# Optimization experiments

Hardware: AMD Instinct MI355X
Metric: run time of the kernel (lower is better)

## Reference

```python
import jax, jax.numpy as jnp
import numpy as np

GAMMA = 2
EPS = 1e-8  # torch F.cosine_similarity norm clamp


def setup_inputs() -> dict:
    key = jax.random.key(0)
    k1, k2, k3 = jax.random.split(key, 3)
    b, c, h, w = 32, 256, 32, 32
    x = jax.random.normal(k1, (b, c, h, w), dtype=jnp.float32)
    # 1x1 conv transform_net (num_layers=1): weight (c_out, c_in), bias (c_out,)
    conv_w = jax.random.normal(k2, (c, c), dtype=jnp.float32) / np.sqrt(c)
    conv_b = jax.random.normal(k3, (c,), dtype=jnp.float32) * 0.01
    return {"x": x, "conv_w": conv_w, "conv_b": conv_b}


def reference(x, conv_w, conv_b):
    b, c, h, w = x.shape
    hw = h * w
    xf = x.reshape(b, c, hw)  # (b, c, hw)
    # cosine similarity: normalize channels once, then a single GEMM
    norm = jnp.sqrt(jnp.sum(xf * xf, axis=1, keepdims=True))
    xn = xf / jnp.maximum(norm, EPS)
    sim = jnp.einsum('bcq,bck->bqk', xn, xn)  # (b, hw, hw)
    sim = jax.nn.relu(sim) ** GAMMA
    # 1x1 conv transform
    t = jnp.einsum('oc,bck->bok', conv_w, xf) + conv_b[None, :, None]  # (b, c, hw)
    # weighted aggregation: out[b, c, q] = sum_k sim[b, q, k] * t[b, c, k]
    out = jnp.einsum('bqk,bck->bcq', sim, t)
    return out.reshape(b, c, h, w)
```

## Files before the change

kernel.cpp:

```cpp
#include <hip/hip_runtime.h>
#include <math.h>

#define B 32
#define C 256
#define HW 1024

typedef __attribute__((ext_vector_type(8))) short bf16x8;
typedef __attribute__((ext_vector_type(4))) float f32x4;

__device__ __forceinline__ unsigned short f2bf(float f) {
    unsigned int u = __float_as_uint(f);
    u += 0x7fffu + ((u >> 16) & 1u);
    return (unsigned short)(u >> 16);
}

__device__ __forceinline__ void gload16(const void* g, void* l) {
    __builtin_amdgcn_global_load_lds(
        (const __attribute__((address_space(1))) unsigned int*)g,
        (__attribute__((address_space(3))) unsigned int*)l, 16, 0, 0);
}

__global__ __launch_bounds__(256) void prepn_kernel(const float* __restrict__ x,
                                                    float* __restrict__ norm,
                                                    unsigned short* __restrict__ xnT) {
    __shared__ float xt[256][65];
    __shared__ float psum[4][64];
    __shared__ float rn[64];
    const int t = threadIdx.x;
    const int q0 = blockIdx.x * 64, b = blockIdx.y;
    const float* xb = x + (size_t)b * C * HW + q0;
#pragma unroll
    for (int p = 0; p < 16; ++p) {
        int u = p * 256 + t;
        int c = u >> 4, q4 = (u & 15) * 4;
        float4 v = *(const float4*)(xb + (size_t)c * HW + q4);
        xt[c][q4] = v.x; xt[c][q4 + 1] = v.y; xt[c][q4 + 2] = v.z; xt[c][q4 + 3] = v.w;
    }
    __syncthreads();
    {
        int cb = t >> 6, q = t & 63;
        float s = 0.f;
#pragma unroll
        for (int cc = 0; cc < 64; ++cc) {
            float v = xt[cb * 64 + cc][q];
            s += v * v;
        }
        psum[cb][q] = s;
    }
    __syncthreads();
    if (t < 64) {
        float s = psum[0][t] + psum[1][t] + psum[2][t] + psum[3][t];
        float n = fmaxf(sqrtf(s), 1e-8f);
        norm[b * HW + q0 + t] = n;
        rn[t] = 1.f / n;
    }
    __syncthreads();
    unsigned short* xrow = xnT + ((size_t)b * HW + q0) * C;
#pragma unroll
    for (int p = 0; p < 16; ++p) {
        int q = p * 4 + (t >> 6);
        float rnq = rn[q];
#pragma unroll
        for (int i = 0; i < 4; ++i) {
            int c = (t & 63) + 64 * i;
            xrow[(size_t)q * C + c] = f2bf(xt[c][q] * rnq);
        }
    }
}

__global__ __launch_bounds__(256) void castw_kernel(const float* __restrict__ w,
                                                    unsigned short* __restrict__ wb) {
    int i = (blockIdx.x * 256 + threadIdx.x) * 4;
    float4 v = *(const float4*)(w + i);
    unsigned long long pk = (unsigned long long)f2bf(v.x) |
                            ((unsigned long long)f2bf(v.y) << 16) |
                            ((unsigned long long)f2bf(v.z) << 32) |
                            ((unsigned long long)f2bf(v.w) << 48);
    *(unsigned long long*)(wb + i) = pk;
}

__global__ __launch_bounds__(256) void tgemm_kernel(
    const unsigned short* __restrict__ A, const unsigned short* __restrict__ Bm,
    unsigned short* __restrict__ Cb, const float* __restrict__ bias,
    const float* __restrict__ norm) {
    __shared__ unsigned short Asub[128 * 64];
    __shared__ unsigned short Bsub[128 * 64];
    const int t = threadIdx.x;
    const int bz = blockIdx.z;
    const int m0 = blockIdx.y * 128, n0 = blockIdx.x * 128;

    const int ug = ((t & 7) ^ ((t >> 3) & 7)) * 16;
    const char* gA = (const char*)A + (size_t)(m0 + (t >> 3)) * (C * 2) + ug;
    const char* gB = (const char*)(Bm + (size_t)bz * HW * C) +
                     (size_t)(n0 + (t >> 3)) * (C * 2) + ug;
    char* lA = (char*)Asub + t * 16;
    char* lB = (char*)Bsub + t * 16;
    const int rowStep = 32 * C * 2;

    const int lane = t & 63;
    const int wid = t >> 6;
    const int wr = wid >> 1, wc = wid & 1;
    const int lr = lane & 15, hi = lane >> 4;
    int rowA[4], rowB[4], sb[2];
#pragma unroll
    for (int i = 0; i < 4; ++i) rowA[i] = (wr * 64 + i * 16 + lr) * 128;
#pragma unroll
    for (int j = 0; j < 4; ++j) rowB[j] = (wc * 64 + j * 16 + lr) * 128;
#pragma unroll
    for (int kk = 0; kk < 2; ++kk) sb[kk] = ((hi + 4 * kk) ^ (lr & 7)) * 16;

    f32x4 acc[4][4];
#pragma unroll
    for (int i = 0; i < 4; ++i)
#pragma unroll
        for (int j = 0; j < 4; ++j) acc[i][j] = (f32x4)(0.f);

#pragma unroll
    for (int p = 0; p < 4; ++p) {
        gload16(gA + p * rowStep, lA + p * 4096);
        gload16(gB + p * rowStep, lB + p * 4096);
    }
    for (int ks = 0; ks < 4; ++ks) {
        __syncthreads();
#pragma unroll
        for (int kk = 0; kk < 2; ++kk) {
            bf16x8 av[4], bv[4];
#pragma unroll
            for (int i = 0; i < 4; ++i)
                av[i] = *(const bf16x8*)((const char*)Asub + rowA[i] + sb[kk]);
#pragma unroll
            for (int j = 0; j < 4; ++j)
                bv[j] = *(const bf16x8*)((const char*)Bsub + rowB[j] + sb[kk]);
#pragma unroll
            for (int i = 0; i < 4; ++i)
#pragma unroll
                for (int j = 0; j < 4; ++j)
                    acc[i][j] = __builtin_amdgcn_mfma_f32_16x16x32_bf16(
                        av[i], bv[j], acc[i][j], 0, 0, 0);
        }
        __syncthreads();
        if (ks + 1 < 4) {
            const char* gA2 = gA + (size_t)(ks + 1) * 128;
            const char* gB2 = gB + (size_t)(ks + 1) * 128;
#pragma unroll
            for (int p = 0; p < 4; ++p) {
                gload16(gA2 + p * rowStep, lA + p * 4096);
                gload16(gB2 + p * rowStep, lB + p * 4096);
            }
        }
    }
    const int mb = m0 + wr * 64 + hi * 4;
    const int nb = n0 + wc * 64 + lr;
    unsigned short* Cp = Cb + (size_t)bz * C * HW;
    float nrm[4];
#pragma unroll
    for (int j = 0; j < 4; ++j) nrm[j] = norm[bz * HW + nb + j * 16];
#pragma unroll
    for (int i = 0; i < 4; ++i)
#pragma unroll
        for (int r = 0; r < 4; ++r) {
            int m = mb + i * 16 + r;
            float bbv = bias[m];
#pragma unroll
            for (int j = 0; j < 4; ++j)
                Cp[(size_t)m * HW + nb + j * 16] = f2bf(acc[i][j][r] * nrm[j] + bbv);
        }
}

__global__ __launch_bounds__(512, 4) void fused_kernel(
    const unsigned short* __restrict__ xnT,
    const unsigned short* __restrict__ tb,
    float* __restrict__ out) {
    __shared__ unsigned short XQ[64 * 256];
    __shared__ unsigned short XK0[128 * 64];
    __shared__ unsigned short XK1[128 * 64];
    __shared__ unsigned short SS[64 * 128];
    const int t = threadIdx.x;
    const int wgid = blockIdx.x;
    const int xcd = wgid & 7, g = wgid >> 3;
    const int qt = g & 15, bh = g >> 4;
    const int b = bh * 8 + xcd;
    const int qg0 = qt * 64;

    const int lane = t & 63;
    const int wid = t >> 6;
    const int lr = lane & 15, hi = lane >> 4;
    const int qh = wid & 1, kq = wid >> 1;

    const char* xq_g = (const char*)(xnT + ((size_t)b * HW + qg0) * C);
    const char* xk_gb = (const char*)(xnT + (size_t)b * HW * C);
    const char* t_gb = (const char*)(tb + (size_t)b * C * HW);

    auto stage_xk = [&](int kg0, int cch, char* dst) {
#pragma unroll
        for (int p = 0; p < 2; ++p) {
            int u = p * 512 + t;
            int k = u >> 3, s = u & 7;
            int sp = s ^ (k & 7);
            gload16(xk_gb + (size_t)(kg0 + k) * 512 + cch * 128 + sp * 16,
                    dst + u * 16);
        }
    };

#pragma unroll
    for (int p = 0; p < 4; ++p) {
        int u = p * 512 + t;
        int q = u >> 5, s = u & 31;
        int sp = (s & 16) | ((s & 15) ^ (q & 15));
        gload16(xq_g + (size_t)q * 512 + sp * 16, (char*)XQ + (size_t)u * 16);
    }
    stage_xk(0, 0, (char*)XK0);

    f32x4 oacc[2][4];
#pragma unroll
    for (int i = 0; i < 2; ++i)
#pragma unroll
        for (int j = 0; j < 4; ++j) oacc[i][j] = (f32x4)(0.f);

    for (int kt = 0; kt < 8; ++kt) {
        const int kg0 = kt * 128;
        f32x4 sacc[2][2];
#pragma unroll
        for (int i = 0; i < 2; ++i)
#pragma unroll
            for (int j = 0; j < 2; ++j) sacc[i][j] = (f32x4)(0.f);

#pragma unroll
        for (int cch = 0; cch < 4; ++cch) {
            __syncthreads();
            char* nbuf = (cch & 1) ? (char*)XK0 : (char*)XK1;
            if (cch < 3) stage_xk(kg0, cch + 1, nbuf);
            else         stage_xk(kt < 7 ? kg0 + 128 : kg0, 0, (char*)XK0);
            const char* xk = (cch & 1) ? (const char*)XK1 : (const char*)XK0;
#pragma unroll
            for (int cs = 0; cs < 2; ++cs) {
                bf16x8 av[2], bv[2];
#pragma unroll
                for (int i = 0; i < 2; ++i) {
                    int krow = kq * 32 + i * 16 + lr;
                    int off = (cs * 64 + hi * 16) ^ ((krow & 7) << 4);
                    av[i] = *(const bf16x8*)(xk + krow * 128 + off);
                }
#pragma unroll
                for (int j = 0; j < 2; ++j) {
                    int qrow = qh * 32 + j * 16 + lr;
                    int off = (cch * 128 + cs * 64 + hi * 16) ^ ((qrow & 15) << 4);
                    bv[j] = *(const bf16x8*)((const char*)XQ + qrow * 512 + off);
                }
#pragma unroll
                for (int i = 0; i < 2; ++i)
#pragma unroll
                    for (int j = 0; j < 2; ++j)
                        sacc[i][j] = __builtin_amdgcn_mfma_f32_16x16x32_bf16(
                            av[i], bv[j], sacc[i][j], 0, 0, 0);
            }
        }

#pragma unroll
        for (int i = 0; i < 2; ++i)
#pragma unroll
            for (int j = 0; j < 2; ++j) {
                int q = qh * 32 + j * 16 + lr;
                int kb = kq * 32 + i * 16 + hi * 4;
                unsigned long long pk = 0;
#pragma unroll
                for (int r = 0; r < 4; ++r) {
                    float v = fmaxf(sacc[i][j][r], 0.f);
                    v = v * v;
                    pk |= (unsigned long long)f2bf(v) << (16 * r);
                }
                int off = (kb * 2) ^ ((q & 15) << 4);
                *(unsigned long long*)((char*)SS + q * 256 + off) = pk;
            }
        __syncthreads();

        bf16x8 tt[2][4];
#pragma unroll
        for (int i = 0; i < 2; ++i)
#pragma unroll
            for (int kc = 0; kc < 4; ++kc)
                tt[i][kc] = *(const bf16x8*)(
                    t_gb + (size_t)(wid * 32 + i * 16 + lr) * 2048 +
                    (kg0 + kc * 32 + hi * 8) * 2);
#pragma unroll
        for (int kc = 0; kc < 4; ++kc) {
            bf16x8 bv[4];
#pragma unroll
            for (int j = 0; j < 4; ++j) {
                int qrow = j * 16 + lr;
                int off = (kc * 64 + hi * 16) ^ ((qrow & 15) << 4);
                bv[j] = *(const bf16x8*)((const char*)SS + qrow * 256 + off);
            }
#pragma unroll
            for (int i = 0; i < 2; ++i)
#pragma unroll
                for (int j = 0; j < 4; ++j)
                    oacc[i][j] = __builtin_amdgcn_mfma_f32_16x16x32_bf16(
                        tt[i][kc], bv[j], oacc[i][j], 0, 0, 0);
        }
    }

#pragma unroll
    for (int i = 0; i < 2; ++i)
#pragma unroll
        for (int r = 0; r < 4; ++r) {
            int c = wid * 32 + i * 16 + hi * 4 + r;
            float* op = out + ((size_t)b * C + c) * HW + qg0 + lr;
#pragma unroll
            for (int j = 0; j < 4; ++j) op[j * 16] = oacc[i][j][r];
        }
}

extern "C" void kernel_launch(void* const* d_in, const int* in_sizes, int n_in,
                              void* d_out, int out_size, void* d_ws, size_t ws_size,
                              hipStream_t stream) {
    const float* x    = (const float*)d_in[0];
    const float* w    = (const float*)d_in[1];
    const float* bias = (const float*)d_in[2];
    float* out = (float*)d_out;

    char* ws = (char*)d_ws;
    float* norm         = (float*)ws;
    unsigned short* wbf = (unsigned short*)(ws + (128 << 10));
    unsigned short* xnT = (unsigned short*)(ws + (256 << 10));
    unsigned short* tb  = (unsigned short*)(ws + (256 << 10) + (16u << 20));

    hipLaunchKernelGGL(prepn_kernel, dim3(HW / 64, B), dim3(256), 0, stream,
                       x, norm, xnT);
    hipLaunchKernelGGL(castw_kernel, dim3(C * C / 1024), dim3(256), 0, stream, w, wbf);
    hipLaunchKernelGGL(tgemm_kernel, dim3(HW / 128, C / 128, B), dim3(256), 0, stream,
                       wbf, xnT, tb, bias, norm);
    hipLaunchKernelGGL(fused_kernel, dim3((HW / 64) * B), dim3(512), 0, stream,
                       xnT, tb, out);
}
```

Before: 78.94 us.

## Load key tiles straight from global into registers, drop LDS double-buffer for keys

The sim GEMM stage no longer stages key rows of xnT through two LDS buffers with per-chunk barriers. Each wave now loads its 16 key rows across all 256 channels directly from global into registers and runs MFMAs against the resident query tile. The work split changes from a 2x4 wave grid to one 16-key slice per wave, and the many __syncthreads are replaced by a few explicit waitcnt+barrier points. This saves LDS space and synchronisation, but adds register pressure and exposes uncoalesced global load latency with no prefetch overlap.

Result: slower. 93.65 us (+18.6%).

```diff
diff --git a/kernel.cpp b/kernel.cpp
--- a/kernel.cpp
+++ b/kernel.cpp
@@ -172,8 +172,6 @@
     const unsigned short* __restrict__ tb,
     float* __restrict__ out) {
     __shared__ unsigned short XQ[64 * 256];
-    __shared__ unsigned short XK0[128 * 64];
-    __shared__ unsigned short XK1[128 * 64];
     __shared__ unsigned short SS[64 * 128];
     const int t = threadIdx.x;
     const int wgid = blockIdx.x;
@@ -185,22 +183,10 @@
     const int lane = t & 63;
     const int wid = t >> 6;
     const int lr = lane & 15, hi = lane >> 4;
-    const int qh = wid & 1, kq = wid >> 1;
 
     const char* xq_g = (const char*)(xnT + ((size_t)b * HW + qg0) * C);
     const char* xk_gb = (const char*)(xnT + (size_t)b * HW * C);
     const char* t_gb = (const char*)(tb + (size_t)b * C * HW);
-
-    auto stage_xk = [&](int kg0, int cch, char* dst) {
-#pragma unroll
-        for (int p = 0; p < 2; ++p) {
-            int u = p * 512 + t;
-            int k = u >> 3, s = u & 7;
-            int sp = s ^ (k & 7);
-            gload16(xk_gb + (size_t)(kg0 + k) * 512 + cch * 128 + sp * 16,
-                    dst + u * 16);
-        }
-    };
 
 #pragma unroll
     for (int p = 0; p < 4; ++p) {
@@ -209,7 +195,9 @@
         int sp = (s & 16) | ((s & 15) ^ (q & 15));
         gload16(xq_g + (size_t)q * 512 + sp * 16, (char*)XQ + (size_t)u * 16);
     }
-    stage_xk(0, 0, (char*)XK0);
+    asm volatile("s_waitcnt vmcnt(0)" ::: "memory");
+    __builtin_amdgcn_sched_barrier(0);
+    __builtin_amdgcn_s_barrier();
 
     f32x4 oacc[2][4];
 #pragma unroll
@@ -219,60 +207,49 @@
 
     for (int kt = 0; kt < 8; ++kt) {
         const int kg0 = kt * 128;
-        f32x4 sacc[2][2];
-#pragma unroll
-        for (int i = 0; i < 2; ++i)
-#pragma unroll
-            for (int j = 0; j < 2; ++j) sacc[i][j] = (f32x4)(0.f);
-
-#pragma unroll
-        for (int cch = 0; cch < 4; ++cch) {
-            __syncthreads();
-            char* nbuf = (cch & 1) ? (char*)XK0 : (char*)XK1;
-            if (cch < 3) stage_xk(kg0, cch + 1, nbuf);
-            else         stage_xk(kt < 7 ? kg0 + 128 : kg0, 0, (char*)XK0);
-            const char* xk = (cch & 1) ? (const char*)XK1 : (const char*)XK0;
-#pragma unroll
-            for (int cs = 0; cs < 2; ++cs) {
-                bf16x8 av[2], bv[2];
-#pragma unroll
-                for (int i = 0; i < 2; ++i) {
-                    int krow = kq * 32 + i * 16 + lr;
-                    int off = (cs * 64 + hi * 16) ^ ((krow & 7) << 4);
-                    av[i] = *(const bf16x8*)(xk + krow * 128 + off);
-                }
-#pragma unroll
-                for (int j = 0; j < 2; ++j) {
-                    int qrow = qh * 32 + j * 16 + lr;
-                    int off = (cch * 128 + cs * 64 + hi * 16) ^ ((qrow & 15) << 4);
-                    bv[j] = *(const bf16x8*)((const char*)XQ + qrow * 512 + off);
-                }
-#pragma unroll
-                for (int i = 0; i < 2; ++i)
-#pragma unroll
-                    for (int j = 0; j < 2; ++j)
-                        sacc[i][j] = __builtin_amdgcn_mfma_f32_16x16x32_bf16(
-                            av[i], bv[j], sacc[i][j], 0, 0, 0);
+
+        const char* avb = xk_gb + (size_t)(kg0 + wid * 16 + lr) * 512 + hi * 16;
+        bf16x8 av[8];
+#pragma unroll
+        for (int cc8 = 0; cc8 < 8; ++cc8)
+            av[cc8] = *(const bf16x8*)(avb + cc8 * 64);
+        f32x4 sacc[4];
+#pragma unroll
+        for (int j = 0; j < 4; ++j) sacc[j] = (f32x4)(0.f);
+#pragma unroll
+        for (int cc8 = 0; cc8 < 8; ++cc8) {
+#pragma unroll
+            for (int j = 0; j < 4; ++j) {
+                int qrow = j * 16 + lr;
+                int off = (cc8 * 64 + hi * 16) ^ ((qrow & 15) << 4);
+                bf16x8 bv = *(const bf16x8*)((const char*)XQ + qrow * 512 + off);
+                sacc[j] = __builtin_amdgcn_mfma_f32_16x16x32_bf16(
+                    av[cc8], bv, sacc[j], 0, 0, 0);
             }
         }
 
-#pragma unroll
-        for (int i = 0; i < 2; ++i)
-#pragma unroll
-            for (int j = 0; j < 2; ++j) {
-                int q = qh * 32 + j * 16 + lr;
-                int kb = kq * 32 + i * 16 + hi * 4;
-                unsigned long long pk = 0;
-#pragma unroll
-                for (int r = 0; r < 4; ++r) {
-                    float v = fmaxf(sacc[i][j][r], 0.f);
-                    v = v * v;
-                    pk |= (unsigned long long)f2bf(v) << (16 * r);
-                }
-                int off = (kb * 2) ^ ((q & 15) << 4);
-                *(unsigned long long*)((char*)SS + q * 256 + off) = pk;
+        asm volatile("s_waitcnt lgkmcnt(0)" ::: "memory");
+        __builtin_amdgcn_sched_barrier(0);
+        __builtin_amdgcn_s_barrier();
+
+#pragma unroll
+        for (int j = 0; j < 4; ++j) {
+            int q = j * 16 + lr;
+            int kb = wid * 16 + hi * 4;
+            unsigned long long pk = 0;
+#pragma unroll
+            for (int r = 0; r < 4; ++r) {
+                float v = fmaxf(sacc[j][r], 0.f);
+                v = v * v;
+                pk |= (unsigned long long)f2bf(v) << (16 * r);
             }
-        __syncthreads();
+            int off = (kb * 2) ^ ((q & 15) << 4);
+            *(unsigned long long*)((char*)SS + q * 256 + off) = pk;
+        }
+
+        asm volatile("s_waitcnt lgkmcnt(0)" ::: "memory");
+        __builtin_amdgcn_sched_barrier(0);
+        __builtin_amdgcn_s_barrier();
 
         bf16x8 tt[2][4];
 #pragma unroll
```
